# Performance work log

Measured on AMD Instinct MI355X. Metric: run time of the kernel, lower is better.

## Reference

```python
import jax, jax.numpy as jnp
import numpy as np

B, F_G, F_L, F_INT = 2, 64, 64, 32
D = H = W = 64
BN_EPS = 1e-5


def setup_inputs() -> dict:
    key = jax.random.key(0)
    ks = jax.random.split(key, 8)
    g = jax.random.normal(ks[0], (B, F_G, D, H, W), dtype=jnp.float32)
    x = jax.random.normal(ks[1], (B, F_L, D, H, W), dtype=jnp.float32)
    # Gating MLP (1x1x1 convs on pooled features == dense layers)
    w1 = jax.random.normal(ks[2], (F_INT, F_G + F_L), dtype=jnp.float32) * (1.0 / np.sqrt(F_G + F_L))
    b1 = jnp.zeros((F_INT,), dtype=jnp.float32)
    w2 = jax.random.normal(ks[3], (F_G * F_L, F_INT), dtype=jnp.float32) * (1.0 / np.sqrt(F_INT))
    b2 = jnp.zeros((F_G * F_L,), dtype=jnp.float32)
    # psi: Conv3d(F_l, 1, k=1) + BatchNorm3d(1) (inference-mode stats)
    psi_w = jax.random.normal(ks[4], (F_L,), dtype=jnp.float32) * (1.0 / np.sqrt(F_L))
    psi_b = jnp.zeros((1,), dtype=jnp.float32)
    bn_gamma = jnp.ones((1,), dtype=jnp.float32)
    bn_beta = jnp.zeros((1,), dtype=jnp.float32)
    bn_mean = jnp.zeros((1,), dtype=jnp.float32)
    bn_var = jnp.ones((1,), dtype=jnp.float32)
    return {"g": g, "x": x, "w1": w1, "b1": b1, "w2": w2, "b2": b2,
            "psi_w": psi_w, "psi_b": psi_b, "bn_gamma": bn_gamma,
            "bn_beta": bn_beta, "bn_mean": bn_mean, "bn_var": bn_var}


def reference(g, x, w1, b1, w2, b2, psi_w, psi_b, bn_gamma, bn_beta, bn_mean, bn_var):
    # Global average pool of cat([g, x]) -> [B, F_g+F_l]
    pooled = jnp.concatenate([jnp.mean(g, axis=(2, 3, 4)), jnp.mean(x, axis=(2, 3, 4))], axis=1)
    h = jax.nn.relu(pooled @ w1.T + b1)                       # [B, F_int]
    dw = jax.nn.sigmoid(h @ w2.T + b2).reshape(B, F_G, F_L)   # dynamic weights [B, F_g, F_l]
    # attended[b,l,d,h,w] = sum_g g[b,g,d,h,w] * dw[b,g,l]  (batched GEMM, no 6D blow-up)
    attended = jnp.einsum('bgdhw,bgl->bldhw', g, dw)
    # psi: 1x1x1 conv to 1 channel + BN + sigmoid
    s = jnp.einsum('bldhw,l->bdhw', attended, psi_w) + psi_b[0]
    s = (s - bn_mean[0]) * (bn_gamma[0] / jnp.sqrt(bn_var[0] + BN_EPS)) + bn_beta[0]
    return x * jax.nn.sigmoid(s)[:, None]                     # [B, F_l, D, H, W]
```

## Files before the change

kernel.cpp:

```cpp
#include <hip/hip_runtime.h>
#include <math.h>

#define SPATIAL (64*64*64)
#define SPATIAL4 (SPATIAL/4)
#define NCH 64
#define NB 2
#define BN_EPS 1e-5f

__global__ __launch_bounds__(512) void mean_kernel(const float* __restrict__ g,
                                                   const float* __restrict__ x,
                                                   float* __restrict__ pooled) {
    int blk = blockIdx.x;
    int tid = threadIdx.x;
    const float* src;
    int outIdx;
    if (blk < 128) {
        int b = blk >> 6, c = blk & 63;
        src = g + (size_t)(b * NCH + c) * SPATIAL;
        outIdx = b * 128 + c;
    } else {
        int id = blk - 128;
        int b = id >> 6, c = id & 63;
        src = x + (size_t)(b * NCH + c) * SPATIAL;
        outIdx = b * 128 + 64 + c;
    }
    const float4* s4 = (const float4*)src;
    float sum = 0.f;
    #pragma unroll 8
    for (int i = tid; i < SPATIAL4; i += 512) {
        float4 v = s4[i];
        sum += (v.x + v.y) + (v.z + v.w);
    }
    #pragma unroll
    for (int off = 32; off > 0; off >>= 1)
        sum += __shfl_down(sum, off, 64);
    __shared__ float wsum[8];
    int lane = tid & 63, wave = tid >> 6;
    if (lane == 0) wsum[wave] = sum;
    __syncthreads();
    if (tid == 0) {
        float t = 0.f;
        #pragma unroll
        for (int w = 0; w < 8; ++w) t += wsum[w];
        pooled[outIdx] = t * (1.0f / SPATIAL);
    }
}

__global__ void mlp_kernel(const float* __restrict__ pooled,
                           const float* __restrict__ w1, const float* __restrict__ b1,
                           const float* __restrict__ w2, const float* __restrict__ b2,
                           const float* __restrict__ psi_w, const float* __restrict__ psi_b,
                           const float* __restrict__ bn_gamma, const float* __restrict__ bn_beta,
                           const float* __restrict__ bn_mean, const float* __restrict__ bn_var,
                           float* __restrict__ coef) {
    __shared__ float p[256];
    __shared__ float h[2][32];
    int tid = threadIdx.x;
    p[tid] = pooled[tid];
    p[tid + 128] = pooled[tid + 128];
    __syncthreads();
    if (tid < 64) {
        int b = tid >> 5, j = tid & 31;
        float acc = b1[j];
        #pragma unroll 8
        for (int k = 0; k < 128; ++k) acc += p[b * 128 + k] * w1[j * 128 + k];
        h[b][j] = fmaxf(acc, 0.f);
    }
    __syncthreads();
    float scale = bn_gamma[0] * rsqrtf(bn_var[0] + BN_EPS);
    {
        int b = tid >> 6, gc = tid & 63;
        float acc = 0.f;
        for (int l = 0; l < 64; ++l) {
            const float* wrow = w2 + (size_t)(gc * 64 + l) * 32;
            float z = b2[gc * 64 + l];
            #pragma unroll 8
            for (int j = 0; j < 32; ++j) z += h[b][j] * wrow[j];
            float sig = 1.f / (1.f + expf(-z));
            acc += sig * psi_w[l];
        }
        coef[tid] = acc * scale;
    }
    if (tid == 0) coef[128] = (psi_b[0] - bn_mean[0]) * scale + bn_beta[0];
}

__global__ __launch_bounds__(256) void apply_kernel(const float* __restrict__ g,
                                                    const float* __restrict__ x,
                                                    const float* __restrict__ coef,
                                                    float* __restrict__ out) {
    int blk = blockIdx.x;
    int batch = blk >> 8;
    int pos4 = (blk & 255) * 256 + threadIdx.x;
    size_t batchOff = (size_t)batch * NCH * SPATIAL4;

    const float4* g4 = (const float4*)g;
    const float4* x4 = (const float4*)x;
    float4* o4 = (float4*)out;

    float4 acc = make_float4(0.f, 0.f, 0.f, 0.f);
    #pragma unroll 16
    for (int gc = 0; gc < NCH; ++gc) {
        float cc = coef[batch * NCH + gc];
        float4 v = g4[batchOff + (size_t)gc * SPATIAL4 + pos4];
        acc.x += v.x * cc; acc.y += v.y * cc;
        acc.z += v.z * cc; acc.w += v.w * cc;
    }
    float d = coef[128];
    float4 sig;
    sig.x = 1.f / (1.f + expf(-(acc.x + d)));
    sig.y = 1.f / (1.f + expf(-(acc.y + d)));
    sig.z = 1.f / (1.f + expf(-(acc.z + d)));
    sig.w = 1.f / (1.f + expf(-(acc.w + d)));

    #pragma unroll 8
    for (int l = 0; l < NCH; ++l) {
        size_t idx = batchOff + (size_t)l * SPATIAL4 + pos4;
        float4 xv = x4[idx];
        float4 ov = make_float4(xv.x * sig.x, xv.y * sig.y, xv.z * sig.z, xv.w * sig.w);
        o4[idx] = ov;
    }
}

extern "C" void kernel_launch(void* const* d_in, const int* in_sizes, int n_in,
                              void* d_out, int out_size, void* d_ws, size_t ws_size,
                              hipStream_t stream) {
    const float* g        = (const float*)d_in[0];
    const float* x        = (const float*)d_in[1];
    const float* w1       = (const float*)d_in[2];
    const float* b1       = (const float*)d_in[3];
    const float* w2       = (const float*)d_in[4];
    const float* b2       = (const float*)d_in[5];
    const float* psi_w    = (const float*)d_in[6];
    const float* psi_b    = (const float*)d_in[7];
    const float* bn_gamma = (const float*)d_in[8];
    const float* bn_beta  = (const float*)d_in[9];
    const float* bn_mean  = (const float*)d_in[10];
    const float* bn_var   = (const float*)d_in[11];
    float* out = (float*)d_out;
    float* ws  = (float*)d_ws;

    float* pooled = ws;
    float* coef   = ws + 256;

    mean_kernel<<<256, 512, 0, stream>>>(g, x, pooled);
    mlp_kernel<<<1, 128, 0, stream>>>(pooled, w1, b1, w2, b2, psi_w, psi_b,
                                      bn_gamma, bn_beta, bn_mean, bn_var, coef);
    apply_kernel<<<512, 256, 0, stream>>>(g, x, coef, out);
}
```

Before: 446.1 us.

## Parallelize mean, MLP and apply kernels across more blocks

The pooling reduction is split into quarter-channel partial sums over 1024 blocks. The gating MLP moves from a single block to 128 blocks, one per (batch, output channel), and reduces the psi dot product with wave shuffles. The apply kernel splits the 64-channel GEMV into two halves per block, combined through shared memory, doubling the grid. This is meant to fix low occupancy and the serial single-block MLP, at the cost of extra shared-memory syncs and a partial-sum buffer.

```diff
diff --git a/kernel.cpp b/kernel.cpp
--- a/kernel.cpp
+++ b/kernel.cpp
@@ -3,50 +3,40 @@
 
 #define SPATIAL (64*64*64)
 #define SPATIAL4 (SPATIAL/4)
+#define QUART4  (SPATIAL4/4)
 #define NCH 64
 #define NB 2
 #define BN_EPS 1e-5f
 
-__global__ __launch_bounds__(512) void mean_kernel(const float* __restrict__ g,
+__global__ __launch_bounds__(256) void mean_kernel(const float* __restrict__ g,
                                                    const float* __restrict__ x,
-                                                   float* __restrict__ pooled) {
+                                                   float* __restrict__ partial) {
     int blk = blockIdx.x;
-    int tid = threadIdx.x;
-    const float* src;
-    int outIdx;
-    if (blk < 128) {
-        int b = blk >> 6, c = blk & 63;
-        src = g + (size_t)(b * NCH + c) * SPATIAL;
-        outIdx = b * 128 + c;
-    } else {
-        int id = blk - 128;
-        int b = id >> 6, c = id & 63;
-        src = x + (size_t)(b * NCH + c) * SPATIAL;
-        outIdx = b * 128 + 64 + c;
-    }
-    const float4* s4 = (const float4*)src;
+    int ch  = blk >> 2;
+    int q   = blk & 3;
+    const float* src = (ch < 128)
+        ? g + (size_t)ch * SPATIAL
+        : x + (size_t)(ch - 128) * SPATIAL;
+    const float4* s4 = (const float4*)src + (size_t)q * QUART4;
+
     float sum = 0.f;
     #pragma unroll 8
-    for (int i = tid; i < SPATIAL4; i += 512) {
+    for (int i = threadIdx.x; i < QUART4; i += 256) {
         float4 v = s4[i];
         sum += (v.x + v.y) + (v.z + v.w);
     }
     #pragma unroll
     for (int off = 32; off > 0; off >>= 1)
         sum += __shfl_down(sum, off, 64);
-    __shared__ float wsum[8];
-    int lane = tid & 63, wave = tid >> 6;
+    __shared__ float wsum[4];
+    int lane = threadIdx.x & 63, wave = threadIdx.x >> 6;
     if (lane == 0) wsum[wave] = sum;
     __syncthreads();
-    if (tid == 0) {
-        float t = 0.f;
-        #pragma unroll
-        for (int w = 0; w < 8; ++w) t += wsum[w];
-        pooled[outIdx] = t * (1.0f / SPATIAL);
-    }
+    if (threadIdx.x == 0)
+        partial[blk] = wsum[0] + wsum[1] + wsum[2] + wsum[3];
 }
 
-__global__ void mlp_kernel(const float* __restrict__ pooled,
+__global__ __launch_bounds__(64) void mlp_kernel(const float* __restrict__ partial,
                            const float* __restrict__ w1, const float* __restrict__ b1,
                            const float* __restrict__ w2, const float* __restrict__ b2,
                            const float* __restrict__ psi_w, const float* __restrict__ psi_b,
@@ -54,70 +44,90 @@
                            const float* __restrict__ bn_mean, const float* __restrict__ bn_var,
                            float* __restrict__ coef) {
     __shared__ float p[256];
-    __shared__ float h[2][32];
+    __shared__ float h[32];
     int tid = threadIdx.x;
-    p[tid] = pooled[tid];
-    p[tid + 128] = pooled[tid + 128];
-    __syncthreads();
-    if (tid < 64) {
-        int b = tid >> 5, j = tid & 31;
-        float acc = b1[j];
-        #pragma unroll 8
-        for (int k = 0; k < 128; ++k) acc += p[b * 128 + k] * w1[j * 128 + k];
-        h[b][j] = fmaxf(acc, 0.f);
+    int blk = blockIdx.x;
+    int b = blk >> 6, gc = blk & 63;
+
+    #pragma unroll
+    for (int ch = tid; ch < 256; ch += 64) {
+        float s = partial[4*ch] + partial[4*ch+1] + partial[4*ch+2] + partial[4*ch+3];
+        int pi = (ch < 128) ? ((ch >> 6) * 128 + (ch & 63))
+                            : (((ch - 128) >> 6) * 128 + 64 + ((ch - 128) & 63));
+        p[pi] = s * (1.0f / SPATIAL);
     }
     __syncthreads();
+    if (tid < 32) {
+        float acc = b1[tid];
+        const float* wr = w1 + tid * 128;
+        #pragma unroll 4
+        for (int k = 0; k < 128; ++k) acc += p[b * 128 + k] * wr[k];
+        h[tid] = fmaxf(acc, 0.f);
+    }
+    __syncthreads();
+    const float4* wr = (const float4*)(w2 + (size_t)(gc * 64 + tid) * 32);
+    float z = b2[gc * 64 + tid];
+    #pragma unroll
+    for (int j = 0; j < 8; ++j) {
+        float4 wv = wr[j];
+        z += h[4*j] * wv.x + h[4*j+1] * wv.y + h[4*j+2] * wv.z + h[4*j+3] * wv.w;
+    }
+    float sig = 1.f / (1.f + expf(-z));
+    float val = sig * psi_w[tid];
+    #pragma unroll
+    for (int off = 32; off > 0; off >>= 1)
+        val += __shfl_down(val, off, 64);
     float scale = bn_gamma[0] * rsqrtf(bn_var[0] + BN_EPS);
-    {
-        int b = tid >> 6, gc = tid & 63;
-        float acc = 0.f;
-        for (int l = 0; l < 64; ++l) {
-            const float* wrow = w2 + (size_t)(gc * 64 + l) * 32;
-            float z = b2[gc * 64 + l];
-            #pragma unroll 8
-            for (int j = 0; j < 32; ++j) z += h[b][j] * wrow[j];
-            float sig = 1.f / (1.f + expf(-z));
-            acc += sig * psi_w[l];
-        }
-        coef[tid] = acc * scale;
-    }
-    if (tid == 0) coef[128] = (psi_b[0] - bn_mean[0]) * scale + bn_beta[0];
+    if (tid == 0) coef[b * 64 + gc] = val * scale;
+    if (blk == 0 && tid == 0)
+        coef[128] = (psi_b[0] - bn_mean[0]) * scale + bn_beta[0];
 }
 
 __global__ __launch_bounds__(256) void apply_kernel(const float* __restrict__ g,
                                                     const float* __restrict__ x,
                                                     const float* __restrict__ coef,
                                                     float* __restrict__ out) {
-    int blk = blockIdx.x;
-    int batch = blk >> 8;
-    int pos4 = (blk & 255) * 256 + threadIdx.x;
-    size_t batchOff = (size_t)batch * NCH * SPATIAL4;
+    int t    = threadIdx.x;
+    int pos  = t & 127;
+    int half = t >> 7;
+    int blk  = blockIdx.x;
+    int batch = blk >> 9;
+    int base4 = (blk & 511) * 128 + pos;
+    size_t bOff = (size_t)batch * NCH * SPATIAL4;
 
     const float4* g4 = (const float4*)g;
     const float4* x4 = (const float4*)x;
     float4* o4 = (float4*)out;
 
+    const float* cf = coef + batch * NCH + half * 32;
     float4 acc = make_float4(0.f, 0.f, 0.f, 0.f);
-    #pragma unroll 16
-    for (int gc = 0; gc < NCH; ++gc) {
-        float cc = coef[batch * NCH + gc];
-        float4 v = g4[batchOff + (size_t)gc * SPATIAL4 + pos4];
+    #pragma unroll 8
+    for (int gc = 0; gc < 32; ++gc) {
+        float cc = cf[gc];
+        float4 v = g4[bOff + (size_t)(half * 32 + gc) * SPATIAL4 + base4];
         acc.x += v.x * cc; acc.y += v.y * cc;
         acc.z += v.z * cc; acc.w += v.w * cc;
     }
-    float d = coef[128];
-    float4 sig;
-    sig.x = 1.f / (1.f + expf(-(acc.x + d)));
-    sig.y = 1.f / (1.f + expf(-(acc.y + d)));
-    sig.z = 1.f / (1.f + expf(-(acc.z + d)));
-    sig.w = 1.f / (1.f + expf(-(acc.w + d)));
-
+    __shared__ float4 red[128];
+    if (half == 1) red[pos] = acc;
+    __syncthreads();
+    if (half == 0) {
+        float4 o = red[pos];
+        float d = coef[128];
+        float4 s;
+        s.x = 1.f / (1.f + expf(-(acc.x + o.x + d)));
+        s.y = 1.f / (1.f + expf(-(acc.y + o.y + d)));
+        s.z = 1.f / (1.f + expf(-(acc.z + o.z + d)));
+        s.w = 1.f / (1.f + expf(-(acc.w + o.w + d)));
+        red[pos] = s;
+    }
+    __syncthreads();
+    float4 s = red[pos];
     #pragma unroll 8
-    for (int l = 0; l < NCH; ++l) {
-        size_t idx = batchOff + (size_t)l * SPATIAL4 + pos4;
+    for (int l = 0; l < 32; ++l) {
+        size_t idx = bOff + (size_t)(half * 32 + l) * SPATIAL4 + base4;
         float4 xv = x4[idx];
-        float4 ov = make_float4(xv.x * sig.x, xv.y * sig.y, xv.z * sig.z, xv.w * sig.w);
-        o4[idx] = ov;
+        o4[idx] = make_float4(xv.x * s.x, xv.y * s.y, xv.z * s.z, xv.w * s.w);
     }
 }
 
@@ -139,11 +149,11 @@
     float* out = (float*)d_out;
     float* ws  = (float*)d_ws;
 
-    float* pooled = ws;
-    float* coef   = ws + 256;
+    float* partial = ws;
+    float* coef    = ws + 1024;
 
-    mean_kernel<<<256, 512, 0, stream>>>(g, x, pooled);
-    mlp_kernel<<<1, 128, 0, stream>>>(pooled, w1, b1, w2, b2, psi_w, psi_b,
-                                      bn_gamma, bn_beta, bn_mean, bn_var, coef);
-    apply_kernel<<<512, 256, 0, stream>>>(g, x, coef, out);
+    mean_kernel<<<1024, 256, 0, stream>>>(g, x, partial);
+    mlp_kernel<<<128, 64, 0, stream>>>(partial, w1, b1, w2, b2, psi_w, psi_b,
+                                       bn_gamma, bn_beta, bn_mean, bn_var, coef);
+    apply_kernel<<<1024, 256, 0, stream>>>(g, x, coef, out);
 }
```

New measurement: 387.1 us. 1.15x faster.
